# Performance work log

Hardware: AMD Instinct MI355X
Metric: run time of the kernel (lower is better)

The kernel has to match this reference:

```python
import jax, jax.numpy as jnp
import numpy as np


def _bce_logits(x, z):
    # numerically stable binary_cross_entropy_with_logits (elementwise)
    return jnp.maximum(x, 0.0) - x * z + jnp.log1p(jnp.exp(-jnp.abs(x)))


def _giou(b1, b2):
    # boxes in (cx, cy, w, h) format, mirrors bbox_iou(..., mode='giou')
    eps = 1e-9
    b1x1 = b1[..., 0] - b1[..., 2] / 2; b1y1 = b1[..., 1] - b1[..., 3] / 2
    b1x2 = b1[..., 0] + b1[..., 2] / 2; b1y2 = b1[..., 1] + b1[..., 3] / 2
    b2x1 = b2[..., 0] - b2[..., 2] / 2; b2y1 = b2[..., 1] - b2[..., 3] / 2
    b2x2 = b2[..., 0] + b2[..., 2] / 2; b2y2 = b2[..., 1] + b2[..., 3] / 2
    a1 = jnp.clip(b1x2 - b1x1, 0.0) * jnp.clip(b1y2 - b1y1, 0.0) + eps
    a2 = jnp.clip(b2x2 - b2x1, 0.0) * jnp.clip(b2y2 - b2y1, 0.0) + eps
    iw = jnp.clip(jnp.minimum(b1x2, b2x2) - jnp.maximum(b1x1, b2x1), 0.0)
    ih = jnp.clip(jnp.minimum(b1y2, b2y2) - jnp.maximum(b1y1, b2y1), 0.0)
    inter = iw * ih + eps
    union = a1 + a2 - inter + eps
    iou = inter / union
    cw = jnp.maximum(b1x2, b2x2) - jnp.minimum(b1x1, b2x1)
    ch = jnp.maximum(b1y2, b2y2) - jnp.minimum(b1y1, b2y1)
    carea = cw * ch + eps
    return iou - (carea - union) / carea


def setup_inputs() -> dict:
    key = jax.random.key(0)
    ks = jax.random.split(key, 8)
    N, A, S, nC, nM, G, H, W = 4, 3, 13, 80, 32, 16, 104, 104
    preds = jax.random.normal(ks[0], (N, A, S, S, 5 + nC + nM), jnp.float32) * 0.5
    prototypes = jax.random.normal(ks[1], (N, nM, H, W), jnp.float32)
    masks = (jax.random.uniform(ks[2], (N, G, H, W)) < 0.3).astype(jnp.float32)
    ii = jnp.arange(S)
    interior = (ii >= 2) & (ii <= 10)
    int2d = interior[:, None] & interior[None, :]
    obj = (jax.random.uniform(ks[3], (N, A, S, S)) < 0.06) & int2d
    obj = obj.at[:, 0, 6, 6].set(True)  # guarantee >= 1 object per image
    xy = jax.random.uniform(ks[4], (N, A, S, S, 2), minval=0.2, maxval=0.8)
    wh = jax.random.uniform(ks[5], (N, A, S, S, 2), minval=0.5, maxval=2.5)
    cls = jax.random.randint(ks[6], (N, A, S, S, 1), 0, nC).astype(jnp.float32)
    mid = jax.random.randint(ks[7], (N, A, S, S, 1), 0, G).astype(jnp.float32)
    target = jnp.concatenate([xy, wh, obj[..., None].astype(jnp.float32), cls, mid], axis=-1)
    anchors = jnp.array([[1.0, 1.5], [2.0, 2.5], [3.5, 3.0]], jnp.float32)
    return {"preds": preds, "target": target, "anchors": anchors,
            "prototypes": prototypes, "masks": masks,
            "num_classes": 80, "num_masks": 32}


def reference(preds, target, anchors, prototypes, masks, num_classes, num_masks):
    eps = 1e-9
    N, A, S = preds.shape[0], preds.shape[1], preds.shape[2]
    H, W = prototypes.shape[2], prototypes.shape[3]
    nC, nM = num_classes, num_masks
    dt = preds.dtype
    conf_t = target[..., 4]
    obj = conf_t == 1.0
    noobj = conf_t == 0.0
    objf = obj.astype(dt)
    noobjf = noobj.astype(dt)
    n_obj = objf.sum()
    n_noobj = noobjf.sum()
    conf_logit = preds[..., 4]
    noobj_loss = (_bce_logits(conf_logit, conf_t) * noobjf).sum() / n_noobj
    # ---- segmentation loss (dense masked equivalent of ragged per-instance crops) ----
    coeffs = jnp.tanh(preds[..., 5 + nC:5 + nC + nM])            # [N,A,S,S,M]
    inst = jnp.einsum('naijm,nmhw->naijhw', coeffs, prototypes)   # instance logits
    cols = jnp.arange(S, dtype=dt)
    # cells_to_boxes: normalized image coords, then scaled to prototype pixels
    bx = (target[..., 0] + cols[None, None, None, :]) / S * W
    by = (target[..., 1] + cols[None, None, :, None]) / S * H
    bw = target[..., 2] / S * W
    bh = target[..., 3] / S * H
    x1 = jnp.floor(bx - bw / 2).astype(jnp.int32)
    x2 = jnp.floor(bx + bw / 2).astype(jnp.int32)
    y1 = jnp.floor(by - bh / 2).astype(jnp.int32)
    y2 = jnp.floor(by + bh / 2).astype(jnp.int32)
    ids = jnp.clip(target[..., 6].astype(jnp.int32), 0, masks.shape[1] - 1)
    tm = masks[jnp.arange(N)[:, None, None, None], ids]           # [N,A,S,S,H,W]
    hh = jnp.arange(H)
    ww = jnp.arange(W)
    rm = ((hh >= y1[..., None]) & (hh < y2[..., None])).astype(dt)  # [N,A,S,S,H]
    cm = ((ww >= x1[..., None]) & (ww < x2[..., None])).astype(dt)  # [N,A,S,S,W]
    bce_el = _bce_logits(inst, tm)
    region_sum = jnp.einsum('naijhw,naijh,naijw->naij', bce_el, rm, cm)
    area = rm.sum(-1) * cm.sum(-1)
    valid = (area > 0) & obj
    seg_mean = jnp.where(valid, region_sum / jnp.maximum(area, 1.0), 0.0)
    segment_loss = seg_mean.sum() / (valid.astype(dt).sum() + eps)
    # ---- box / obj / class losses ----
    anch = anchors.reshape(1, A, 1, 1, 2)
    pred_box = jnp.concatenate([jax.nn.sigmoid(preds[..., 0:2]),
                                jnp.exp(preds[..., 2:4]) * anch], axis=-1)
    giou = _giou(pred_box, target[..., 0:4])                      # [N,A,S,S]
    obj_tgt = conf_t * jnp.clip(jax.lax.stop_gradient(giou), 0.0)
    obj_loss = (_bce_logits(conf_logit, obj_tgt) * objf).sum() / n_obj
    # note: original applies BCEWithLogits to sigmoid(xy) (double squash) - faithful
    xy_bce = (_bce_logits(jax.nn.sigmoid(preds[..., 0:2]), target[..., 0:2])
              * objf[..., None]).sum() / (n_obj * 2)
    twh = jnp.log(1e-16 + target[..., 2:4] / anch)
    wh_mse = (((preds[..., 2:4] - twh) ** 2) * objf[..., None]).sum() / (n_obj * 2)
    box_loss = xy_bce + wh_mse + ((1.0 - giou) * objf).sum() / n_obj
    logp = jax.nn.log_softmax(preds[..., 5:5 + nC], axis=-1)
    labels = target[..., 5].astype(jnp.int32)
    nll = -jnp.take_along_axis(logp, labels[..., None], axis=-1)[..., 0]
    class_loss = (nll * objf).sum() / n_obj
    box_l = 8.0 * box_loss
    obj_l = 2.0 * obj_loss
    noobj_l = 4.0 * noobj_loss
    cls_l = 1.0 * class_loss
    seg_l = 10.0 * segment_loss
    total = box_l + obj_l + noobj_l + cls_l + seg_l
    return jnp.stack([box_l, obj_l, noobj_l, cls_l, seg_l, total])
```

## Files before the change

kernel.cpp:

```cpp
#include <hip/hip_runtime.h>
#include <math.h>

#define N_  4
#define A_  3
#define S_  13
#define NC_ 80
#define NM_ 32
#define G_  16
#define H_  104
#define W_  104
#define CH_ (5 + NC_ + NM_)
#define HW_ (H_ * W_)
#define NCELL (N_ * A_ * S_ * S_)

#define MAIN_BLOCKS 64
#define PROW 16

__device__ __forceinline__ float bce_logits(float x, float z) {
    return fmaxf(x, 0.0f) - x * z + log1pf(expf(-fabsf(x)));
}

__device__ __forceinline__ float sigmoidf(float x) {
    return 1.0f / (1.0f + expf(-x));
}

__device__ __forceinline__ float giou_fn(float cx1, float cy1, float w1, float h1,
                                         float cx2, float cy2, float w2, float h2) {
    const float eps = 1e-9f;
    float b1x1 = cx1 - w1 * 0.5f, b1y1 = cy1 - h1 * 0.5f;
    float b1x2 = cx1 + w1 * 0.5f, b1y2 = cy1 + h1 * 0.5f;
    float b2x1 = cx2 - w2 * 0.5f, b2y1 = cy2 - h2 * 0.5f;
    float b2x2 = cx2 + w2 * 0.5f, b2y2 = cy2 + h2 * 0.5f;
    float a1 = fmaxf(b1x2 - b1x1, 0.0f) * fmaxf(b1y2 - b1y1, 0.0f) + eps;
    float a2 = fmaxf(b2x2 - b2x1, 0.0f) * fmaxf(b2y2 - b2y1, 0.0f) + eps;
    float iw = fmaxf(fminf(b1x2, b2x2) - fmaxf(b1x1, b2x1), 0.0f);
    float ih = fmaxf(fminf(b1y2, b2y2) - fmaxf(b1y1, b2y1), 0.0f);
    float inter = iw * ih + eps;
    float uni   = a1 + a2 - inter + eps;
    float iou   = inter / uni;
    float cw = fmaxf(b1x2, b2x2) - fminf(b1x1, b2x1);
    float ch = fmaxf(b1y2, b2y2) - fminf(b1y1, b2y1);
    float carea = cw * ch + eps;
    return iou - (carea - uni) / carea;
}

__device__ __forceinline__ int region_bounds(const float* t, int i, int j,
                                             int& lox, int& loy, int& ncols, int& nrows) {
    float bx = (t[0] + (float)j) * ((float)W_ / (float)S_);
    float by = (t[1] + (float)i) * ((float)H_ / (float)S_);
    float bw = t[2] * ((float)W_ / (float)S_);
    float bh = t[3] * ((float)H_ / (float)S_);
    int x1 = (int)floorf(bx - bw * 0.5f);
    int x2 = (int)floorf(bx + bw * 0.5f);
    int y1 = (int)floorf(by - bh * 0.5f);
    int y2 = (int)floorf(by + bh * 0.5f);
    lox = max(x1, 0); loy = max(y1, 0);
    ncols = max(min(x2, W_) - lox, 0);
    nrows = max(min(y2, H_) - loy, 0);
    return nrows * ncols;
}

__global__ __launch_bounds__(256) void yolo_main_kernel(
    const float* __restrict__ preds,
    const float* __restrict__ target,
    const float* __restrict__ anchors,
    const float* __restrict__ protos,
    const float* __restrict__ masks,
    float* __restrict__ partials)
{
    const int b   = blockIdx.x;
    const int tid = threadIdx.x;

    __shared__ float s_tc[NM_];
    __shared__ float s_w[4][8];
    __shared__ float s_red[4];
    __shared__ int   s_list[40];
    __shared__ int   s_nvalid;

    if (b < 8) {
        const int cell = b * 256 + tid;
        float v0 = 0.f, v1 = 0.f, v2 = 0.f, v3 = 0.f,
              v4 = 0.f, v5 = 0.f, v6 = 0.f, v7 = 0.f;

        if (cell < NCELL) {
            const int a = (cell / (S_ * S_)) % A_;
            const float* t = target + (size_t)cell * 7;
            const float* p = preds  + (size_t)cell * CH_;
            const float conf_t = t[4];
            const float x = p[4];

            if (conf_t == 0.0f) {
                v1 = 1.0f;
                v2 = bce_logits(x, 0.0f);
            } else if (conf_t == 1.0f) {
                v0 = 1.0f;
                float tx = t[0], ty = t[1], tw = t[2], th = t[3];
                float aw = anchors[a * 2 + 0], ah = anchors[a * 2 + 1];
                float sx = sigmoidf(p[0]);
                float sy = sigmoidf(p[1]);
                float pw = expf(p[2]) * aw;
                float ph = expf(p[3]) * ah;
                float giou = giou_fn(sx, sy, pw, ph, tx, ty, tw, th);
                v3 = bce_logits(x, fmaxf(giou, 0.0f));
                v4 = bce_logits(sx, tx) + bce_logits(sy, ty);
                float twl = logf(1e-16f + tw / aw);
                float thl = logf(1e-16f + th / ah);
                float dw = p[2] - twl, dh = p[3] - thl;
                v5 = dw * dw + dh * dh;
                v6 = 1.0f - giou;

                float mx = -1e30f;
                #pragma unroll 8
                for (int c = 0; c < NC_; ++c) mx = fmaxf(mx, p[5 + c]);
                float se = 0.0f;
                #pragma unroll 8
                for (int c = 0; c < NC_; ++c) se += expf(p[5 + c] - mx);
                int label = (int)t[5];
                v7 = (mx + logf(se)) - p[5 + label];
            }
        }

        #pragma unroll
        for (int o = 32; o > 0; o >>= 1) {
            v0 += __shfl_xor(v0, o, 64);  v1 += __shfl_xor(v1, o, 64);
            v2 += __shfl_xor(v2, o, 64);  v3 += __shfl_xor(v3, o, 64);
            v4 += __shfl_xor(v4, o, 64);  v5 += __shfl_xor(v5, o, 64);
            v6 += __shfl_xor(v6, o, 64);  v7 += __shfl_xor(v7, o, 64);
        }
        if ((tid & 63) == 0) {
            int w = tid >> 6;
            s_w[w][0] = v0; s_w[w][1] = v1; s_w[w][2] = v2; s_w[w][3] = v3;
            s_w[w][4] = v4; s_w[w][5] = v5; s_w[w][6] = v6; s_w[w][7] = v7;
        }
        __syncthreads();
        if (tid < 8) {
            partials[b * PROW + tid] =
                s_w[0][tid] + s_w[1][tid] + s_w[2][tid] + s_w[3][tid];
        }
        __syncthreads();
    }

    if (tid == 0) s_nvalid = 0;
    __syncthreads();
    if (tid < 32) {
        int c = tid * 64 + b;
        if (c < NCELL) {
            const float* t = target + (size_t)c * 7;
            if (t[4] == 1.0f) {
                int lox, loy, ncols, nrows;
                int area = region_bounds(t, (c / S_) % S_, c % S_,
                                         lox, loy, ncols, nrows);
                if (area > 0) {
                    int k = atomicAdd(&s_nvalid, 1);
                    s_list[k] = c;
                }
            }
        }
    }
    __syncthreads();
    const int nv = s_nvalid;
    float block_seg = 0.0f;

    for (int ii = 0; ii < nv; ++ii) {
        const int cell = s_list[ii];
        const int j = cell % S_;
        const int i = (cell / S_) % S_;
        const int n = cell / (A_ * S_ * S_);
        const float* t = target + (size_t)cell * 7;
        const float* p = preds  + (size_t)cell * CH_;

        int lox, loy, ncols, nrows;
        int area = region_bounds(t, i, j, lox, loy, ncols, nrows);

        if (tid < NM_) s_tc[tid] = tanhf(p[5 + NC_ + tid]);
        __syncthreads();

        int id = (int)t[6];
        id = min(max(id, 0), G_ - 1);
        const float* tm = masks  + ((size_t)(n * G_ + id)) * HW_;
        const float* pr = protos + (size_t)n * NM_ * HW_;

        float lsum = 0.0f;
        for (int px = tid; px < area; px += 256) {
            int h = loy + px / ncols;
            int w = lox + px % ncols;
            int off = h * W_ + w;
            float inst = 0.0f;
            #pragma unroll
            for (int m = 0; m < NM_; ++m)
                inst += s_tc[m] * pr[m * HW_ + off];
            lsum += bce_logits(inst, tm[off]);
        }

        #pragma unroll
        for (int o = 32; o > 0; o >>= 1) lsum += __shfl_xor(lsum, o, 64);
        if ((tid & 63) == 0) s_red[tid >> 6] = lsum;
        __syncthreads();
        if (tid == 0) {
            float tot = s_red[0] + s_red[1] + s_red[2] + s_red[3];
            block_seg += tot / fmaxf((float)area, 1.0f);
        }
        __syncthreads();
    }

    if (tid == 0) {
        partials[b * PROW + 8] = block_seg;
        partials[b * PROW + 9] = (float)nv;
    }
}

__global__ __launch_bounds__(64) void yolo_finalize_kernel(
    const float* __restrict__ partials,
    float* __restrict__ out)
{
    const int t = threadIdx.x;
    float s0 = 0.f, s1 = 0.f, s2 = 0.f, s3 = 0.f,
          s4 = 0.f, s5 = 0.f, s6 = 0.f, s7 = 0.f, s8 = 0.f, s9 = 0.f;
    if (t < 8) {
        s0 = partials[t * PROW + 0]; s1 = partials[t * PROW + 1];
        s2 = partials[t * PROW + 2]; s3 = partials[t * PROW + 3];
        s4 = partials[t * PROW + 4]; s5 = partials[t * PROW + 5];
        s6 = partials[t * PROW + 6]; s7 = partials[t * PROW + 7];
    }
    s8 = partials[t * PROW + 8];
    s9 = partials[t * PROW + 9];

    #pragma unroll
    for (int o = 32; o > 0; o >>= 1) {
        s0 += __shfl_xor(s0, o, 64);  s1 += __shfl_xor(s1, o, 64);
        s2 += __shfl_xor(s2, o, 64);  s3 += __shfl_xor(s3, o, 64);
        s4 += __shfl_xor(s4, o, 64);  s5 += __shfl_xor(s5, o, 64);
        s6 += __shfl_xor(s6, o, 64);  s7 += __shfl_xor(s7, o, 64);
        s8 += __shfl_xor(s8, o, 64);  s9 += __shfl_xor(s9, o, 64);
    }

    if (t == 0) {
        float n_obj   = s0;
        float n_noobj = s1;
        float noobj_loss = s2 / n_noobj;
        float obj_loss   = s3 / n_obj;
        float xy_bce     = s4 / (n_obj * 2.0f);
        float wh_mse     = s5 / (n_obj * 2.0f);
        float box_loss   = xy_bce + wh_mse + s6 / n_obj;
        float class_loss = s7 / n_obj;
        float seg_loss   = s8 / (s9 + 1e-9f);
        float box_l   = 8.0f * box_loss;
        float obj_l   = 2.0f * obj_loss;
        float noobj_l = 4.0f * noobj_loss;
        float cls_l   = 1.0f * class_loss;
        float seg_l   = 10.0f * seg_loss;
        out[0] = box_l;
        out[1] = obj_l;
        out[2] = noobj_l;
        out[3] = cls_l;
        out[4] = seg_l;
        out[5] = box_l + obj_l + noobj_l + cls_l + seg_l;
    }
}

extern "C" void kernel_launch(void* const* d_in, const int* in_sizes, int n_in,
                              void* d_out, int out_size, void* d_ws, size_t ws_size,
                              hipStream_t stream) {
    const float* preds   = (const float*)d_in[0];
    const float* target  = (const float*)d_in[1];
    const float* anchors = (const float*)d_in[2];
    const float* protos  = (const float*)d_in[3];
    const float* masks   = (const float*)d_in[4];

    float* partials = (float*)d_ws;
    float* out      = (float*)d_out;

    yolo_main_kernel<<<MAIN_BLOCKS, 256, 0, stream>>>(preds, target, anchors,
                                                      protos, masks, partials);
    yolo_finalize_kernel<<<1, 64, 0, stream>>>(partials, out);
}
```

Measured before the change: 95.81 us.

## Fuse finalize into main kernel via last-block ticket; per-wave segment objects

Removes the separate finalize launch: each block bumps a self-wrapping atomicInc ticket, and the last block reduces the partials and writes the outputs. The segment loop now gives each of the four waves its own object instead of running all 256 threads on one object. Mask coefficients are broadcast with readlane into registers, which removes the shared-memory staging and the block barriers inside the loop. This costs more registers for the 32 coefficients and serialises an object's pixels within one wave, and it depends on the workspace ticket starting at zero.

After: 98.17 us. 1.02x slower.

```diff
diff --git a/kernel.cpp b/kernel.cpp
--- a/kernel.cpp
+++ b/kernel.cpp
@@ -22,6 +22,10 @@
 
 __device__ __forceinline__ float sigmoidf(float x) {
     return 1.0f / (1.0f + expf(-x));
+}
+
+__device__ __forceinline__ float readlane_f(float v, int l) {
+    return __int_as_float(__builtin_amdgcn_readlane(__float_as_int(v), l));
 }
 
 __device__ __forceinline__ float giou_fn(float cx1, float cy1, float w1, float h1,
@@ -60,22 +64,26 @@
     return nrows * ncols;
 }
 
-__global__ __launch_bounds__(256) void yolo_main_kernel(
+__global__ __launch_bounds__(256) void yolo_fused_kernel(
     const float* __restrict__ preds,
     const float* __restrict__ target,
     const float* __restrict__ anchors,
     const float* __restrict__ protos,
     const float* __restrict__ masks,
-    float* __restrict__ partials)
+    float* __restrict__ partials,
+    unsigned int* __restrict__ ticket,
+    float* __restrict__ out)
 {
-    const int b   = blockIdx.x;
-    const int tid = threadIdx.x;
-
-    __shared__ float s_tc[NM_];
+    const int b    = blockIdx.x;
+    const int tid  = threadIdx.x;
+    const int wav  = tid >> 6;
+    const int lane = tid & 63;
+
     __shared__ float s_w[4][8];
     __shared__ float s_red[4];
     __shared__ int   s_list[40];
     __shared__ int   s_nvalid;
+    __shared__ int   s_last;
 
     if (b < 8) {
         const int cell = b * 256 + tid;
@@ -137,7 +145,6 @@
             partials[b * PROW + tid] =
                 s_w[0][tid] + s_w[1][tid] + s_w[2][tid] + s_w[3][tid];
         }
-        __syncthreads();
     }
 
     if (tid == 0) s_nvalid = 0;
@@ -159,9 +166,9 @@
     }
     __syncthreads();
     const int nv = s_nvalid;
-    float block_seg = 0.0f;
-
-    for (int ii = 0; ii < nv; ++ii) {
+
+    float wave_seg = 0.0f;
+    for (int ii = wav; ii < nv; ii += 4) {
         const int cell = s_list[ii];
         const int j = cell % S_;
         const int i = (cell / S_) % S_;
@@ -170,10 +177,14 @@
         const float* p = preds  + (size_t)cell * CH_;
 
         int lox, loy, ncols, nrows;
-        int area = region_bounds(t, i, j, lox, loy, ncols, nrows);
-
-        if (tid < NM_) s_tc[tid] = tanhf(p[5 + NC_ + tid]);
-        __syncthreads();
+        region_bounds(t, i, j, lox, loy, ncols, nrows);
+        const int area = nrows * ncols;
+
+        float cv = 0.0f;
+        if (lane < NM_) cv = tanhf(p[5 + NC_ + lane]);
+        float cm[NM_];
+        #pragma unroll
+        for (int m = 0; m < NM_; ++m) cm[m] = readlane_f(cv, m);
 
         int id = (int)t[6];
         id = min(max(id, 0), G_ - 1);
@@ -181,80 +192,83 @@
         const float* pr = protos + (size_t)n * NM_ * HW_;
 
         float lsum = 0.0f;
-        for (int px = tid; px < area; px += 256) {
+        for (int px = lane; px < area; px += 64) {
             int h = loy + px / ncols;
             int w = lox + px % ncols;
             int off = h * W_ + w;
             float inst = 0.0f;
             #pragma unroll
             for (int m = 0; m < NM_; ++m)
-                inst += s_tc[m] * pr[m * HW_ + off];
+                inst += cm[m] * pr[m * HW_ + off];
             lsum += bce_logits(inst, tm[off]);
         }
 
         #pragma unroll
         for (int o = 32; o > 0; o >>= 1) lsum += __shfl_xor(lsum, o, 64);
-        if ((tid & 63) == 0) s_red[tid >> 6] = lsum;
-        __syncthreads();
-        if (tid == 0) {
-            float tot = s_red[0] + s_red[1] + s_red[2] + s_red[3];
-            block_seg += tot / fmaxf((float)area, 1.0f);
-        }
-        __syncthreads();
-    }
-
+        if (lane == 0) wave_seg += lsum / fmaxf((float)area, 1.0f);
+    }
+
+    if (lane == 0) s_red[wav] = wave_seg;
+    __syncthreads();
     if (tid == 0) {
-        partials[b * PROW + 8] = block_seg;
+        partials[b * PROW + 8] = s_red[0] + s_red[1] + s_red[2] + s_red[3];
         partials[b * PROW + 9] = (float)nv;
     }
-}
-
-__global__ __launch_bounds__(64) void yolo_finalize_kernel(
-    const float* __restrict__ partials,
-    float* __restrict__ out)
-{
-    const int t = threadIdx.x;
-    float s0 = 0.f, s1 = 0.f, s2 = 0.f, s3 = 0.f,
-          s4 = 0.f, s5 = 0.f, s6 = 0.f, s7 = 0.f, s8 = 0.f, s9 = 0.f;
-    if (t < 8) {
-        s0 = partials[t * PROW + 0]; s1 = partials[t * PROW + 1];
-        s2 = partials[t * PROW + 2]; s3 = partials[t * PROW + 3];
-        s4 = partials[t * PROW + 4]; s5 = partials[t * PROW + 5];
-        s6 = partials[t * PROW + 6]; s7 = partials[t * PROW + 7];
-    }
-    s8 = partials[t * PROW + 8];
-    s9 = partials[t * PROW + 9];
-
-    #pragma unroll
-    for (int o = 32; o > 0; o >>= 1) {
-        s0 += __shfl_xor(s0, o, 64);  s1 += __shfl_xor(s1, o, 64);
-        s2 += __shfl_xor(s2, o, 64);  s3 += __shfl_xor(s3, o, 64);
-        s4 += __shfl_xor(s4, o, 64);  s5 += __shfl_xor(s5, o, 64);
-        s6 += __shfl_xor(s6, o, 64);  s7 += __shfl_xor(s7, o, 64);
-        s8 += __shfl_xor(s8, o, 64);  s9 += __shfl_xor(s9, o, 64);
-    }
-
-    if (t == 0) {
-        float n_obj   = s0;
-        float n_noobj = s1;
-        float noobj_loss = s2 / n_noobj;
-        float obj_loss   = s3 / n_obj;
-        float xy_bce     = s4 / (n_obj * 2.0f);
-        float wh_mse     = s5 / (n_obj * 2.0f);
-        float box_loss   = xy_bce + wh_mse + s6 / n_obj;
-        float class_loss = s7 / n_obj;
-        float seg_loss   = s8 / (s9 + 1e-9f);
-        float box_l   = 8.0f * box_loss;
-        float obj_l   = 2.0f * obj_loss;
-        float noobj_l = 4.0f * noobj_loss;
-        float cls_l   = 1.0f * class_loss;
-        float seg_l   = 10.0f * seg_loss;
-        out[0] = box_l;
-        out[1] = obj_l;
-        out[2] = noobj_l;
-        out[3] = cls_l;
-        out[4] = seg_l;
-        out[5] = box_l + obj_l + noobj_l + cls_l + seg_l;
+
+    __threadfence();
+    __syncthreads();
+    if (tid == 0) {
+        unsigned int old = atomicInc(ticket, MAIN_BLOCKS - 1u);
+        s_last = (old == MAIN_BLOCKS - 2u) ? 1 : 0;
+    }
+    __syncthreads();
+    if (!s_last) return;
+
+    __threadfence();
+    if (tid < 64) {
+        const int t = tid;
+        float s0 = 0.f, s1 = 0.f, s2 = 0.f, s3 = 0.f,
+              s4 = 0.f, s5 = 0.f, s6 = 0.f, s7 = 0.f, s8 = 0.f, s9 = 0.f;
+        if (t < 8) {
+            s0 = partials[t * PROW + 0]; s1 = partials[t * PROW + 1];
+            s2 = partials[t * PROW + 2]; s3 = partials[t * PROW + 3];
+            s4 = partials[t * PROW + 4]; s5 = partials[t * PROW + 5];
+            s6 = partials[t * PROW + 6]; s7 = partials[t * PROW + 7];
+        }
+        s8 = partials[t * PROW + 8];
+        s9 = partials[t * PROW + 9];
+
+        #pragma unroll
+        for (int o = 32; o > 0; o >>= 1) {
+            s0 += __shfl_xor(s0, o, 64);  s1 += __shfl_xor(s1, o, 64);
+            s2 += __shfl_xor(s2, o, 64);  s3 += __shfl_xor(s3, o, 64);
+            s4 += __shfl_xor(s4, o, 64);  s5 += __shfl_xor(s5, o, 64);
+            s6 += __shfl_xor(s6, o, 64);  s7 += __shfl_xor(s7, o, 64);
+            s8 += __shfl_xor(s8, o, 64);  s9 += __shfl_xor(s9, o, 64);
+        }
+
+        if (t == 0) {
+            float n_obj   = s0;
+            float n_noobj = s1;
+            float noobj_loss = s2 / n_noobj;
+            float obj_loss   = s3 / n_obj;
+            float xy_bce     = s4 / (n_obj * 2.0f);
+            float wh_mse     = s5 / (n_obj * 2.0f);
+            float box_loss   = xy_bce + wh_mse + s6 / n_obj;
+            float class_loss = s7 / n_obj;
+            float seg_loss   = s8 / (s9 + 1e-9f);
+            float box_l   = 8.0f * box_loss;
+            float obj_l   = 2.0f * obj_loss;
+            float noobj_l = 4.0f * noobj_loss;
+            float cls_l   = 1.0f * class_loss;
+            float seg_l   = 10.0f * seg_loss;
+            out[0] = box_l;
+            out[1] = obj_l;
+            out[2] = noobj_l;
+            out[3] = cls_l;
+            out[4] = seg_l;
+            out[5] = box_l + obj_l + noobj_l + cls_l + seg_l;
+        }
     }
 }
 
@@ -267,10 +281,11 @@
     const float* protos  = (const float*)d_in[3];
     const float* masks   = (const float*)d_in[4];
 
-    float* partials = (float*)d_ws;
-    float* out      = (float*)d_out;
-
-    yolo_main_kernel<<<MAIN_BLOCKS, 256, 0, stream>>>(preds, target, anchors,
-                                                      protos, masks, partials);
-    yolo_finalize_kernel<<<1, 64, 0, stream>>>(partials, out);
-}
+    float* partials      = (float*)d_ws;
+    unsigned int* ticket = (unsigned int*)(partials + MAIN_BLOCKS * PROW);
+    float* out           = (float*)d_out;
+
+    yolo_fused_kernel<<<MAIN_BLOCKS, 256, 0, stream>>>(preds, target, anchors,
+                                                       protos, masks, partials,
+                                                       ticket, out);
+}
```

## Assign segmentation objects per wavefront instead of per block

Applied to the files above, without the earlier changes.

The segment-loss phase now splits objects across individual wavefronts (256 global waves, 8 cells each) instead of whole blocks. Each wave picks its valid objects with a ballot and handles each object's mask region on its own. Mask coefficients are computed with tanh in lanes and broadcast into registers with readlane, which removes the shared-memory staging and the block-wide syncs for every object. The trade-off is that each object now gets only 64 threads instead of 256, so large regions run longer on a single wave, but waves no longer stall on each other.

Measured after the change: 94.94 us. About the same (-0.9%).

```diff
diff --git a/kernel.cpp b/kernel.cpp
--- a/kernel.cpp
+++ b/kernel.cpp
@@ -22,6 +22,10 @@
 
 __device__ __forceinline__ float sigmoidf(float x) {
     return 1.0f / (1.0f + expf(-x));
+}
+
+__device__ __forceinline__ float readlane_f(float v, int l) {
+    return __int_as_float(__builtin_amdgcn_readlane(__float_as_int(v), l));
 }
 
 __device__ __forceinline__ float giou_fn(float cx1, float cy1, float w1, float h1,
@@ -44,12 +48,13 @@
     return iou - (carea - uni) / carea;
 }
 
-__device__ __forceinline__ int region_bounds(const float* t, int i, int j,
-                                             int& lox, int& loy, int& ncols, int& nrows) {
-    float bx = (t[0] + (float)j) * ((float)W_ / (float)S_);
-    float by = (t[1] + (float)i) * ((float)H_ / (float)S_);
-    float bw = t[2] * ((float)W_ / (float)S_);
-    float bh = t[3] * ((float)H_ / (float)S_);
+__device__ __forceinline__ int region_bounds_v(float t0, float t1, float t2, float t3,
+                                               int i, int j,
+                                               int& lox, int& loy, int& ncols, int& nrows) {
+    float bx = (t0 + (float)j) * ((float)W_ / (float)S_);
+    float by = (t1 + (float)i) * ((float)H_ / (float)S_);
+    float bw = t2 * ((float)W_ / (float)S_);
+    float bh = t3 * ((float)H_ / (float)S_);
     int x1 = (int)floorf(bx - bw * 0.5f);
     int x2 = (int)floorf(bx + bw * 0.5f);
     int y1 = (int)floorf(by - bh * 0.5f);
@@ -68,14 +73,14 @@
     const float* __restrict__ masks,
     float* __restrict__ partials)
 {
-    const int b   = blockIdx.x;
-    const int tid = threadIdx.x;
-
-    __shared__ float s_tc[NM_];
+    const int b    = blockIdx.x;
+    const int tid  = threadIdx.x;
+    const int wav  = tid >> 6;
+    const int lane = tid & 63;
+
     __shared__ float s_w[4][8];
-    __shared__ float s_red[4];
-    __shared__ int   s_list[40];
-    __shared__ int   s_nvalid;
+    __shared__ float s_seg[4];
+    __shared__ int   s_nv[4];
 
     if (b < 8) {
         const int cell = b * 256 + tid;
@@ -137,43 +142,43 @@
             partials[b * PROW + tid] =
                 s_w[0][tid] + s_w[1][tid] + s_w[2][tid] + s_w[3][tid];
         }
-        __syncthreads();
-    }
-
-    if (tid == 0) s_nvalid = 0;
-    __syncthreads();
-    if (tid < 32) {
-        int c = tid * 64 + b;
-        if (c < NCELL) {
-            const float* t = target + (size_t)c * 7;
-            if (t[4] == 1.0f) {
-                int lox, loy, ncols, nrows;
-                int area = region_bounds(t, (c / S_) % S_, c % S_,
-                                         lox, loy, ncols, nrows);
-                if (area > 0) {
-                    int k = atomicAdd(&s_nvalid, 1);
-                    s_list[k] = c;
-                }
-            }
-        }
-    }
-    __syncthreads();
-    const int nv = s_nvalid;
-    float block_seg = 0.0f;
-
-    for (int ii = 0; ii < nv; ++ii) {
-        const int cell = s_list[ii];
+    }
+
+    const int gw = b * 4 + wav;
+
+    unsigned long long vmask;
+    {
+        int   c  = gw + (lane << 8);
+        bool  in = (lane < 8) && (c < NCELL);
+        float conf = 0.0f;
+        if (in) conf = target[(size_t)c * 7 + 4];
+        vmask = __ballot(in && conf == 1.0f);
+    }
+
+    float wave_seg = 0.0f;
+    int   wave_nv  = 0;
+    while (vmask) {
+        const int l = __ffsll(vmask) - 1;
+        vmask &= vmask - 1;
+        const int cell = gw + (l << 8);
         const int j = cell % S_;
         const int i = (cell / S_) % S_;
         const int n = cell / (A_ * S_ * S_);
         const float* t = target + (size_t)cell * 7;
         const float* p = preds  + (size_t)cell * CH_;
 
+        float t0 = t[0], t1 = t[1], t2 = t[2], t3 = t[3];
         int lox, loy, ncols, nrows;
-        int area = region_bounds(t, i, j, lox, loy, ncols, nrows);
-
-        if (tid < NM_) s_tc[tid] = tanhf(p[5 + NC_ + tid]);
-        __syncthreads();
+        region_bounds_v(t0, t1, t2, t3, i, j, lox, loy, ncols, nrows);
+        const int area = nrows * ncols;
+        if (area <= 0) continue;
+        wave_nv++;
+
+        float cv = 0.0f;
+        if (lane < NM_) cv = tanhf(p[5 + NC_ + lane]);
+        float cm[NM_];
+        #pragma unroll
+        for (int m = 0; m < NM_; ++m) cm[m] = readlane_f(cv, m);
 
         int id = (int)t[6];
         id = min(max(id, 0), G_ - 1);
@@ -181,31 +186,27 @@
         const float* pr = protos + (size_t)n * NM_ * HW_;
 
         float lsum = 0.0f;
-        for (int px = tid; px < area; px += 256) {
+        for (int px = lane; px < area; px += 64) {
             int h = loy + px / ncols;
             int w = lox + px % ncols;
             int off = h * W_ + w;
             float inst = 0.0f;
             #pragma unroll
             for (int m = 0; m < NM_; ++m)
-                inst += s_tc[m] * pr[m * HW_ + off];
+                inst += cm[m] * pr[m * HW_ + off];
             lsum += bce_logits(inst, tm[off]);
         }
 
         #pragma unroll
         for (int o = 32; o > 0; o >>= 1) lsum += __shfl_xor(lsum, o, 64);
-        if ((tid & 63) == 0) s_red[tid >> 6] = lsum;
-        __syncthreads();
-        if (tid == 0) {
-            float tot = s_red[0] + s_red[1] + s_red[2] + s_red[3];
-            block_seg += tot / fmaxf((float)area, 1.0f);
-        }
-        __syncthreads();
-    }
-
+        if (lane == 0) wave_seg += lsum / (float)area;
+    }
+
+    if (lane == 0) { s_seg[wav] = wave_seg; s_nv[wav] = wave_nv; }
+    __syncthreads();
     if (tid == 0) {
-        partials[b * PROW + 8] = block_seg;
-        partials[b * PROW + 9] = (float)nv;
+        partials[b * PROW + 8] = s_seg[0] + s_seg[1] + s_seg[2] + s_seg[3];
+        partials[b * PROW + 9] = (float)(s_nv[0] + s_nv[1] + s_nv[2] + s_nv[3]);
     }
 }
 
```
